# Kernel optimization log

Measured on AMD Instinct MI355X. Metric: run time of the kernel, lower is better.

## Reference

```python
import jax, jax.numpy as jnp
import numpy as np

N_EMBED = 288
HEAD_SIZE = 32


def setup_inputs() -> dict:
    key = jax.random.key(0)
    kx, kk, kq, kv = jax.random.split(key, 4)
    B, T, C = 16, 2048, N_EMBED
    scale = 1.0 / np.sqrt(C)
    return {
        "x": jax.random.normal(kx, (B, T, C), dtype=jnp.float32),
        # Linear(n_embed, head_size, bias=False) weights, stored as [C, head_size]
        "Wk": jax.random.normal(kk, (C, HEAD_SIZE), dtype=jnp.float32) * scale,
        "Wq": jax.random.normal(kq, (C, HEAD_SIZE), dtype=jnp.float32) * scale,
        "Wv": jax.random.normal(kv, (C, HEAD_SIZE), dtype=jnp.float32) * scale,
    }


def reference(x, Wk, Wq, Wv):
    # x: [B, T, C]
    k = x @ Wk  # [B, T, hs]
    q = x @ Wq
    v = x @ Wv
    # NOTE: source computes k @ q^T (not q @ k^T) -- reproduce faithfully.
    weights = jnp.einsum("bth,bsh->bts", k, q) * (HEAD_SIZE ** -0.5)  # [B, T, T]
    T = x.shape[1]
    causal = jnp.tril(jnp.ones((T, T), dtype=bool))
    weights = jnp.where(causal, weights, -jnp.inf)
    weights = jax.nn.softmax(weights, axis=-1)
    return weights @ v  # [B, T, hs]
```

## Files before the change

### kernel.cpp

```cpp
#include <hip/hip_runtime.h>

typedef __bf16 bf16;
typedef __attribute__((ext_vector_type(8))) __bf16 bf16x8;
typedef __attribute__((ext_vector_type(4))) float f32x4;

#define BATCH 16
#define SEQ   2048
#define CEMB  288
#define HS    32
#define NROWS (BATCH * SEQ)

#define XSTR 296

__global__ __launch_bounds__(384) void proj_kernel(
    const float* __restrict__ x, const float* __restrict__ Wk,
    const float* __restrict__ Wq, const float* __restrict__ Wv,
    bf16* __restrict__ Kx, bf16* __restrict__ Qm, bf16* __restrict__ VT)
{
    __shared__ __align__(16) bf16 Xl[32 * XSTR];

    const int tid  = threadIdx.x;
    const int wv   = tid >> 6;
    const int lane = tid & 63;
    const int quad = lane >> 4;
    const int ln   = lane & 15;
    const int dsel = wv >> 1;
    const int half = wv & 1;

    const float SCALE = 0.25519486439582695f;

    const float* Wsrc = (dsel == 0) ? Wk : ((dsel == 1) ? Wq : Wv);
    const float mul = (dsel == 0) ? SCALE : 1.0f;
    bf16x8 wfrag[9];
    for (int kc = 0; kc < 9; ++kc) {
        bf16x8 f;
#pragma unroll
        for (int j = 0; j < 8; ++j) {
            float w = Wsrc[(kc * 32 + quad * 8 + j) * HS + half * 16 + ln];
            f[j] = (bf16)(w * mul);
        }
        wfrag[kc] = f;
    }

    const int wgRowBase = blockIdx.x * 128;
    for (int it = 0; it < 4; ++it) {
        __syncthreads();
        const int rb = wgRowBase + it * 32;
#pragma unroll
        for (int i = 0; i < 6; ++i) {
            int f = tid + 384 * i;
            int row = f / 72;
            int c4  = f - row * 72;
            f32x4 v = ((const f32x4*)x)[(rb + row) * 72 + c4];
            bf16* d = &Xl[row * XSTR + c4 * 4];
            d[0] = (bf16)v[0]; d[1] = (bf16)v[1];
            d[2] = (bf16)v[2]; d[3] = (bf16)v[3];
        }
        __syncthreads();

#pragma unroll
        for (int m = 0; m < 2; ++m) {
            f32x4 acc = {0.f, 0.f, 0.f, 0.f};
#pragma unroll
            for (int kc = 0; kc < 9; ++kc) {
                bf16x8 a = *(const bf16x8*)&Xl[(m * 16 + ln) * XSTR + kc * 32 + quad * 8];
                acc = __builtin_amdgcn_mfma_f32_16x16x32_bf16(a, wfrag[kc], acc, 0, 0, 0);
            }
#pragma unroll
            for (int reg = 0; reg < 4; ++reg) {
                int gr = rb + m * 16 + quad * 4 + reg;
                bf16 val = (bf16)acc[reg];
                if (dsel == 0) {
                    Kx[gr * HS + half * 16 + ln] = val;
                } else if (dsel == 1) {
                    Qm[gr * HS + half * 16 + ln] = val;
                } else {
                    VT[(gr >> 11) * (HS * SEQ) + (half * 16 + ln) * SEQ + (gr & 2047)] = val;
                }
            }
        }
    }
}

#define QSTR 40
#define PSTR 56

__constant__ unsigned char MAP_TILE[40] = {
    4,5,6,7, 8,8,9,9, 10,10,11,11, 12,12,12, 13,13,13, 14,14,14, 15,15,15,
    3,7,11,15, 2,6,10,14, 1,5,9,13, 0,4,8,12 };
__constant__ unsigned char MAP_CHUNK[40] = {
    0,0,0,0, 0,1,0,1, 0,1,0,1, 0,1,2, 0,1,2, 0,1,2, 0,1,2,
    0,1,2,3, 0,1,2,3, 0,1,2,3, 0,1,2,3 };

__global__ __launch_bounds__(256) void attn_kernel(
    const bf16* __restrict__ Kx, const bf16* __restrict__ Qm,
    const bf16* __restrict__ VT,
    float* __restrict__ Opart, float* __restrict__ Lpart)
{
    __shared__ __align__(16) bf16 qT[32 * QSTR];
    __shared__ __align__(16) bf16 vT[32 * QSTR];
    __shared__ __align__(16) bf16 Pl[4][2][16 * PSTR];

    const int tid  = threadIdx.x;
    const int w    = tid >> 6;
    const int lane = tid & 63;
    const int quad = lane >> 4;
    const int ln   = lane & 15;

    const int bid   = blockIdx.x;
    const int b     = bid & 15;
    const int u     = bid >> 4;
    const int tile  = MAP_TILE[u];
    const int chunk = MAP_CHUNK[u];
    const int t0    = tile * 128;
    const int cs    = chunk * 512;
    const int ce    = min(cs + 512, t0 + 128);

    const bf16* Kb = Kx + b * SEQ * HS;
    const bf16* Qb = Qm + b * SEQ * HS;
    const bf16* Vb = VT + b * HS * SEQ;

    int tsub[2];
    bf16x8 kfrag[2];
#pragma unroll
    for (int m = 0; m < 2; ++m) {
        tsub[m] = t0 + w * 32 + m * 16;
        kfrag[m] = *(const bf16x8*)&Kb[(tsub[m] + ln) * HS + quad * 8];
    }
    bf16x8 ones;
#pragma unroll
    for (int j = 0; j < 8; ++j) ones[j] = (bf16)1.0f;

    f32x4 Of[2][2] = {};
    f32x4 Lf[2]    = {};

    for (int s0 = cs; s0 < ce; s0 += 32) {
        __syncthreads();
        if (tid < 128) {
            int sr = tid >> 2, h8 = (tid & 3) * 8;
            *(bf16x8*)&qT[sr * QSTR + h8] = *(const bf16x8*)&Qb[(s0 + sr) * HS + h8];
        } else {
            int t2 = tid - 128;
            int hr = t2 >> 2, s8 = (t2 & 3) * 8;
            *(bf16x8*)&vT[hr * QSTR + s8] = *(const bf16x8*)&Vb[hr * SEQ + s0 + s8];
        }
        __syncthreads();

#pragma unroll
        for (int m = 0; m < 2; ++m) {
            if (s0 >= tsub[m] + 16) continue;
            const bool diag = (s0 + 31 > tsub[m]);

            f32x4 S[2];
#pragma unroll
            for (int ss = 0; ss < 2; ++ss) {
                bf16x8 qf = *(const bf16x8*)&qT[(ss * 16 + ln) * QSTR + quad * 8];
                f32x4 z = {0.f, 0.f, 0.f, 0.f};
                S[ss] = __builtin_amdgcn_mfma_f32_16x16x32_bf16(kfrag[m], qf, z, 0, 0, 0);
            }

            bf16* P = &Pl[w][m][0];
#pragma unroll
            for (int ss = 0; ss < 2; ++ss) {
#pragma unroll
                for (int reg = 0; reg < 4; ++reg) {
                    float p = __builtin_amdgcn_exp2f(S[ss][reg]);
                    if (diag) {
                        int s = s0 + ss * 16 + ln;
                        int t = tsub[m] + quad * 4 + reg;
                        p = (s <= t) ? p : 0.0f;
                    }
                    P[(quad * 4 + reg) * PSTR + ss * 16 + ln] = (bf16)p;
                }
            }

            bf16x8 ap = *(const bf16x8*)&P[ln * PSTR + quad * 8];
            bf16x8 v0 = *(const bf16x8*)&vT[ln * QSTR + quad * 8];
            bf16x8 v1 = *(const bf16x8*)&vT[(16 + ln) * QSTR + quad * 8];
            Of[m][0] = __builtin_amdgcn_mfma_f32_16x16x32_bf16(ap, v0, Of[m][0], 0, 0, 0);
            Of[m][1] = __builtin_amdgcn_mfma_f32_16x16x32_bf16(ap, v1, Of[m][1], 0, 0, 0);
            Lf[m]    = __builtin_amdgcn_mfma_f32_16x16x32_bf16(ap, ones, Lf[m], 0, 0, 0);
        }
    }

#pragma unroll
    for (int m = 0; m < 2; ++m) {
        if (cs >= tsub[m] + 16) continue;
#pragma unroll
        for (int reg = 0; reg < 4; ++reg) {
            int gr = b * SEQ + tsub[m] + quad * 4 + reg;
            float* od = Opart + ((size_t)chunk * NROWS + gr) * HS;
            od[ln]      = Of[m][0][reg];
            od[16 + ln] = Of[m][1][reg];
            if (ln == 0) Lpart[chunk * NROWS + gr] = Lf[m][reg];
        }
    }
}

__global__ __launch_bounds__(256) void combine_kernel(
    const float* __restrict__ Opart, const float* __restrict__ Lpart,
    float* __restrict__ out)
{
    int idx = blockIdx.x * 256 + threadIdx.x;
    int gr = idx >> 3, h4 = idx & 7;
    int t  = gr & 2047;
    int nc = (t >> 9) + 1;
    f32x4 acc = {0.f, 0.f, 0.f, 0.f};
    float l = 0.f;
    for (int c = 0; c < nc; ++c) {
        acc += ((const f32x4*)Opart)[((size_t)c * NROWS + gr) * 8 + h4];
        l   += Lpart[c * NROWS + gr];
    }
    f32x4 r = acc / l;
    ((f32x4*)out)[idx] = r;
}

extern "C" void kernel_launch(void* const* d_in, const int* in_sizes, int n_in,
                              void* d_out, int out_size, void* d_ws, size_t ws_size,
                              hipStream_t stream) {
    (void)in_sizes; (void)n_in; (void)out_size; (void)ws_size;
    const float* x  = (const float*)d_in[0];
    const float* Wk = (const float*)d_in[1];
    const float* Wq = (const float*)d_in[2];
    const float* Wv = (const float*)d_in[3];

    char* ws = (char*)d_ws;
    bf16*  Kx    = (bf16*)(ws);
    bf16*  Qm    = (bf16*)(ws + 2097152);
    bf16*  VT    = (bf16*)(ws + 4194304);
    float* Opart = (float*)(ws + 6291456);
    float* Lpart = (float*)(ws + 23068672);
    float* out   = (float*)d_out;

    hipLaunchKernelGGL(proj_kernel, dim3(256), dim3(384), 0, stream,
                       x, Wk, Wq, Wv, Kx, Qm, VT);
    hipLaunchKernelGGL(attn_kernel, dim3(640), dim3(256), 0, stream,
                       Kx, Qm, VT, Opart, Lpart);
    hipLaunchKernelGGL(combine_kernel, dim3(1024), dim3(256), 0, stream,
                       Opart, Lpart, out);
}
```

Baseline: 112.1 us.

## Split attention into finer KV chunks, load Q/V fragments directly from global

The attention split-K chunk shrinks from 512 to 256 keys, and a new tile/chunk map launches 1152 blocks instead of 640. Each iteration now handles 64 keys, with Q and V fragments read straight from global memory into registers, so the LDS staging and its two barriers per step are gone. Fully masked 16-key subtiles are skipped. The projection kernel uses twice as many smaller blocks, occupancy hints are added, and the batch index is permuted across blocks. The finer split doubles the partial-output traffic and the work in the combine pass, in exchange for better load balance and no block-level syncs.

```diff
diff --git a/kernel.cpp b/kernel.cpp
--- a/kernel.cpp
+++ b/kernel.cpp
@@ -12,7 +12,7 @@
 
 #define XSTR 296
 
-__global__ __launch_bounds__(384) void proj_kernel(
+__global__ __launch_bounds__(384, 3) void proj_kernel(
     const float* __restrict__ x, const float* __restrict__ Wk,
     const float* __restrict__ Wq, const float* __restrict__ Wv,
     bf16* __restrict__ Kx, bf16* __restrict__ Qm, bf16* __restrict__ VT)
@@ -42,8 +42,8 @@
         wfrag[kc] = f;
     }
 
-    const int wgRowBase = blockIdx.x * 128;
-    for (int it = 0; it < 4; ++it) {
+    const int wgRowBase = blockIdx.x * 64;
+    for (int it = 0; it < 2; ++it) {
         __syncthreads();
         const int rb = wgRowBase + it * 32;
 #pragma unroll
@@ -82,23 +82,48 @@
     }
 }
 
-#define QSTR 40
-#define PSTR 56
-
-__constant__ unsigned char MAP_TILE[40] = {
-    4,5,6,7, 8,8,9,9, 10,10,11,11, 12,12,12, 13,13,13, 14,14,14, 15,15,15,
-    3,7,11,15, 2,6,10,14, 1,5,9,13, 0,4,8,12 };
-__constant__ unsigned char MAP_CHUNK[40] = {
-    0,0,0,0, 0,1,0,1, 0,1,0,1, 0,1,2, 0,1,2, 0,1,2, 0,1,2,
-    0,1,2,3, 0,1,2,3, 0,1,2,3, 0,1,2,3 };
-
-__global__ __launch_bounds__(256) void attn_kernel(
+#define PSTR 72
+
+__constant__ unsigned char MAP_TILE[72] = {
+    15,15,15,15,15,15,15,
+    14,14,14,14,14,14,14,
+    13,13,13,13,13,13,
+    12,12,12,12,12,12,
+    11,11,11,11,11,
+    10,10,10,10,10,
+    9,9,9,9,
+    8,8,8,8,
+    7,7,7,
+    6,6,6,
+    5,5,
+    4,4,
+    3,
+    2,
+    15,13,11,9,7,5,3,1,
+    14,12,10,8,6,4,2,0 };
+__constant__ unsigned char MAP_CHUNK[72] = {
+    0,1,2,3,4,5,6,
+    0,1,2,3,4,5,6,
+    0,1,2,3,4,5,
+    0,1,2,3,4,5,
+    0,1,2,3,4,
+    0,1,2,3,4,
+    0,1,2,3,
+    0,1,2,3,
+    0,1,2,
+    0,1,2,
+    0,1,
+    0,1,
+    0,
+    0,
+    7,6,5,4,3,2,1,0,
+    7,6,5,4,3,2,1,0 };
+
+__global__ __launch_bounds__(256, 4) void attn_kernel(
     const bf16* __restrict__ Kx, const bf16* __restrict__ Qm,
     const bf16* __restrict__ VT,
     float* __restrict__ Opart, float* __restrict__ Lpart)
 {
-    __shared__ __align__(16) bf16 qT[32 * QSTR];
-    __shared__ __align__(16) bf16 vT[32 * QSTR];
     __shared__ __align__(16) bf16 Pl[4][2][16 * PSTR];
 
     const int tid  = threadIdx.x;
@@ -108,13 +133,13 @@
     const int ln   = lane & 15;
 
     const int bid   = blockIdx.x;
-    const int b     = bid & 15;
     const int u     = bid >> 4;
+    const int b     = ((bid & 7) << 1) | ((bid >> 3) & 1);
     const int tile  = MAP_TILE[u];
     const int chunk = MAP_CHUNK[u];
     const int t0    = tile * 128;
-    const int cs    = chunk * 512;
-    const int ce    = min(cs + 512, t0 + 128);
+    const int cs    = chunk * 256;
+    const int ce    = min(cs + 256, t0 + 128);
 
     const bf16* Kb = Kx + b * SEQ * HS;
     const bf16* Qb = Qm + b * SEQ * HS;
@@ -134,38 +159,40 @@
     f32x4 Of[2][2] = {};
     f32x4 Lf[2]    = {};
 
-    for (int s0 = cs; s0 < ce; s0 += 32) {
-        __syncthreads();
-        if (tid < 128) {
-            int sr = tid >> 2, h8 = (tid & 3) * 8;
-            *(bf16x8*)&qT[sr * QSTR + h8] = *(const bf16x8*)&Qb[(s0 + sr) * HS + h8];
-        } else {
-            int t2 = tid - 128;
-            int hr = t2 >> 2, s8 = (t2 & 3) * 8;
-            *(bf16x8*)&vT[hr * QSTR + s8] = *(const bf16x8*)&Vb[hr * SEQ + s0 + s8];
-        }
-        __syncthreads();
+    for (int s0 = cs; s0 < ce; s0 += 64) {
+        if (s0 >= tsub[1] + 16) break;
+
+        bf16x8 qf[4];
+#pragma unroll
+        for (int ss = 0; ss < 4; ++ss)
+            qf[ss] = *(const bf16x8*)&Qb[(s0 + ss * 16 + ln) * HS + quad * 8];
+        bf16x8 vf[2][2];
+#pragma unroll
+        for (int hb = 0; hb < 2; ++hb)
+#pragma unroll
+            for (int kb = 0; kb < 2; ++kb)
+                vf[hb][kb] = *(const bf16x8*)&Vb[(hb * 16 + ln) * SEQ + s0 + kb * 32 + quad * 8];
 
 #pragma unroll
         for (int m = 0; m < 2; ++m) {
             if (s0 >= tsub[m] + 16) continue;
-            const bool diag = (s0 + 31 > tsub[m]);
-
-            f32x4 S[2];
-#pragma unroll
-            for (int ss = 0; ss < 2; ++ss) {
-                bf16x8 qf = *(const bf16x8*)&qT[(ss * 16 + ln) * QSTR + quad * 8];
+            const bool diagstep = (s0 + 63 > tsub[m]);
+            bf16* P = &Pl[w][m][0];
+
+#pragma unroll
+            for (int ss = 0; ss < 4; ++ss) {
+                if (s0 + ss * 16 > tsub[m] + 15) {
+#pragma unroll
+                    for (int reg = 0; reg < 4; ++reg)
+                        P[(quad * 4 + reg) * PSTR + ss * 16 + ln] = (bf16)0.0f;
+                    continue;
+                }
                 f32x4 z = {0.f, 0.f, 0.f, 0.f};
-                S[ss] = __builtin_amdgcn_mfma_f32_16x16x32_bf16(kfrag[m], qf, z, 0, 0, 0);
-            }
-
-            bf16* P = &Pl[w][m][0];
-#pragma unroll
-            for (int ss = 0; ss < 2; ++ss) {
+                f32x4 S = __builtin_amdgcn_mfma_f32_16x16x32_bf16(kfrag[m], qf[ss], z, 0, 0, 0);
 #pragma unroll
                 for (int reg = 0; reg < 4; ++reg) {
-                    float p = __builtin_amdgcn_exp2f(S[ss][reg]);
-                    if (diag) {
+                    float p = __builtin_amdgcn_exp2f(S[reg]);
+                    if (diagstep) {
                         int s = s0 + ss * 16 + ln;
                         int t = tsub[m] + quad * 4 + reg;
                         p = (s <= t) ? p : 0.0f;
@@ -174,12 +201,16 @@
                 }
             }
 
-            bf16x8 ap = *(const bf16x8*)&P[ln * PSTR + quad * 8];
-            bf16x8 v0 = *(const bf16x8*)&vT[ln * QSTR + quad * 8];
-            bf16x8 v1 = *(const bf16x8*)&vT[(16 + ln) * QSTR + quad * 8];
-            Of[m][0] = __builtin_amdgcn_mfma_f32_16x16x32_bf16(ap, v0, Of[m][0], 0, 0, 0);
-            Of[m][1] = __builtin_amdgcn_mfma_f32_16x16x32_bf16(ap, v1, Of[m][1], 0, 0, 0);
-            Lf[m]    = __builtin_amdgcn_mfma_f32_16x16x32_bf16(ap, ones, Lf[m], 0, 0, 0);
+            bf16x8 ap0 = *(const bf16x8*)&P[ln * PSTR + quad * 8];
+            Of[m][0] = __builtin_amdgcn_mfma_f32_16x16x32_bf16(ap0, vf[0][0], Of[m][0], 0, 0, 0);
+            Of[m][1] = __builtin_amdgcn_mfma_f32_16x16x32_bf16(ap0, vf[1][0], Of[m][1], 0, 0, 0);
+            Lf[m]    = __builtin_amdgcn_mfma_f32_16x16x32_bf16(ap0, ones,    Lf[m],    0, 0, 0);
+            if (s0 + 32 <= tsub[m] + 15) {
+                bf16x8 ap1 = *(const bf16x8*)&P[ln * PSTR + 32 + quad * 8];
+                Of[m][0] = __builtin_amdgcn_mfma_f32_16x16x32_bf16(ap1, vf[0][1], Of[m][0], 0, 0, 0);
+                Of[m][1] = __builtin_amdgcn_mfma_f32_16x16x32_bf16(ap1, vf[1][1], Of[m][1], 0, 0, 0);
+                Lf[m]    = __builtin_amdgcn_mfma_f32_16x16x32_bf16(ap1, ones,    Lf[m],    0, 0, 0);
+            }
         }
     }
 
@@ -204,7 +235,7 @@
     int idx = blockIdx.x * 256 + threadIdx.x;
     int gr = idx >> 3, h4 = idx & 7;
     int t  = gr & 2047;
-    int nc = (t >> 9) + 1;
+    int nc = (t >> 8) + 1;
     f32x4 acc = {0.f, 0.f, 0.f, 0.f};
     float l = 0.f;
     for (int c = 0; c < nc; ++c) {
@@ -229,12 +260,12 @@
     bf16*  Qm    = (bf16*)(ws + 2097152);
     bf16*  VT    = (bf16*)(ws + 4194304);
     float* Opart = (float*)(ws + 6291456);
-    float* Lpart = (float*)(ws + 23068672);
+    float* Lpart = (float*)(ws + 6291456 + 33554432);
     float* out   = (float*)d_out;
 
-    hipLaunchKernelGGL(proj_kernel, dim3(256), dim3(384), 0, stream,
+    hipLaunchKernelGGL(proj_kernel, dim3(512), dim3(384), 0, stream,
                        x, Wk, Wq, Wv, Kx, Qm, VT);
-    hipLaunchKernelGGL(attn_kernel, dim3(640), dim3(256), 0, stream,
+    hipLaunchKernelGGL(attn_kernel, dim3(1152), dim3(256), 0, stream,
                        Kx, Qm, VT, Opart, Lpart);
     hipLaunchKernelGGL(combine_kernel, dim3(1024), dim3(256), 0, stream,
                        Opart, Lpart, out);
```

Result: faster. 109.8 us (-2.1%).
